# Performance work log

Measured on AMD Instinct MI355X. Metric: run time of the kernel, lower is better.

## Reference

```python
import jax, jax.numpy as jnp
import numpy as np
from jax import lax

N_ITER = 5
SMOOTHNESS_WEIGHT = 1.0
SMOOTHNESS_THETA = 1.0
FILTER_SIZE = 11  # crfseg-style default odd Gaussian filter size


def _gaussian_kernel_1d():
    c = (FILTER_SIZE - 1) / 2.0
    d = jnp.arange(FILTER_SIZE, dtype=jnp.float32) - c
    k = jnp.exp(-(d ** 2) / (2.0 * SMOOTHNESS_THETA ** 2))
    return k / jnp.sum(k)


def _blur(q):
    # q: (B, C, H, W); separable per-channel Gaussian smoothing, 'same' padding
    B, C, H, W = q.shape
    k = _gaussian_kernel_1d()
    r = q.reshape(B * C, 1, H, W)
    dn = ('NCHW', 'OIHW', 'NCHW')
    r = lax.conv_general_dilated(r, k.reshape(1, 1, FILTER_SIZE, 1), (1, 1), 'SAME', dimension_numbers=dn)
    r = lax.conv_general_dilated(r, k.reshape(1, 1, 1, FILTER_SIZE), (1, 1), 'SAME', dimension_numbers=dn)
    return r.reshape(B, C, H, W)


def setup_inputs() -> dict:
    key = jax.random.key(0)
    k1, k2 = jax.random.split(key)
    x = jax.random.normal(k1, (16, 3, 512, 512), dtype=jnp.float32)
    conv_w = jax.random.normal(k2, (2, 3, 3, 3), dtype=jnp.float32) * 0.1
    conv_b = jnp.zeros((2,), dtype=jnp.float32)
    return {"x": x, "conv_w": conv_w, "conv_b": conv_b}


def reference(x, conv_w, conv_b):
    # backbone: simple 3x3 conv producing per-class logits (B, C, H, W)
    dn = ('NCHW', 'OIHW', 'NCHW')
    logits = lax.conv_general_dilated(x, conv_w, (1, 1), 'SAME', dimension_numbers=dn)
    logits = logits + conv_b[None, :, None, None]

    # mean-field CRF: compatibility mu(k,k') = -(k==k') => message = -blur(q)
    unary = logits
    cur = logits
    for _ in range(N_ITER):
        q = jax.nn.softmax(cur, axis=1)
        cur = unary + SMOOTHNESS_WEIGHT * _blur(q)
    return cur
```

## Files before the change

### kernel.cpp

```cpp
#include <hip/hip_runtime.h>

constexpr int BB = 16;
constexpr int HH = 512;
constexpr int WW = 512;
constexpr int HW = HH * WW;
constexpr int NP1 = BB * HW;

using half_t = _Float16;
using half2v = __attribute__((ext_vector_type(2))) _Float16;
using half8v = __attribute__((ext_vector_type(8))) _Float16;

__device__ __forceinline__ half2v hfma2(half2v a, half2v b, half2v c) {
#if __has_builtin(__builtin_elementwise_fma)
    return __builtin_elementwise_fma(a, b, c);
#else
    return a * b + c;
#endif
}

__device__ constexpr float GK[11] = {
    1.4867195147342977e-06f,
    1.3383022576488537e-04f,
    4.4318484119380075e-03f,
    5.3990966513188063e-02f,
    2.4197072451914337e-01f,
    3.9894228040143270e-01f,
    2.4197072451914337e-01f,
    5.3990966513188063e-02f,
    4.4318484119380075e-03f,
    1.3383022576488537e-04f,
    1.4867195147342977e-06f,
};
__device__ constexpr float PFX[6] = {
    0.0f,
    1.4867195147342977e-06f,
    1.3531694527962e-04f,
    4.5671653572176e-03f,
    5.8558131870406e-02f,
    3.0052885638955e-01f,
};

__device__ __forceinline__ float edgeS(int i) {
    float s = 1.f;
    if (i < 5)   s -= PFX[5 - i];
    if (i > 506) s -= PFX[i - 506];
    return s;
}

__device__ __forceinline__ float sig1(float d) {
    d = fminf(fmaxf(d, -30.f), 30.f);
    float e = __expf(d);
    return e * __builtin_amdgcn_rcpf(1.f + e);
}

__device__ __forceinline__ half2v hblur_pk(const half_t* vr, int tid) {
    const unsigned int* vd = (const unsigned int*)vr;
    unsigned int D[7];
#pragma unroll
    for (int k = 0; k < 7; ++k) D[k] = vd[tid + k];
    half2v m01 = half2v{(half_t)0.f, (half_t)0.f};
#pragma unroll
    for (int t = 0; t < 11; ++t) {
        unsigned int P;
        if (t & 1) P = D[(t + 1) >> 1];
        else       P = (D[t >> 1] >> 16) | (D[(t >> 1) + 1] << 16);
        half2v Ph = __builtin_bit_cast(half2v, P);
        half_t kh = (half_t)GK[t];
        half2v kv = half2v{kh, kh};
        m01 = hfma2(kv, Ph, m01);
    }
    return m01;
}

__global__ __launch_bounds__(256) void conv3x3_duq(
    const float* __restrict__ x, const float* __restrict__ w,
    const float* __restrict__ bias, half_t* __restrict__ u0p,
    half_t* __restrict__ dup, half_t* __restrict__ q0p)
{
    int bid = blockIdx.x;
    int sb  = (bid & 7) * 128 + (bid >> 3);
    int t   = sb * 256 + threadIdx.x;
    int b   = t >> 14;
    int rem = t & 16383;
    int y0  = (rem >> 6) << 1;
    int xs  = (rem & 63) << 3;

    float W[54];
#pragma unroll
    for (int i = 0; i < 13; ++i)
        *(float4*)&W[4 * i] = *(const float4*)(w + 4 * i);
    W[52] = w[52];
    W[53] = w[53];
    float b0 = bias[0], b1 = bias[1];

    float acc0[2][8], acc1[2][8];
#pragma unroll
    for (int r = 0; r < 2; ++r)
#pragma unroll
        for (int j = 0; j < 8; ++j) { acc0[r][j] = b0; acc1[r][j] = b1; }

    const float* xb = x + (size_t)b * 3 * HW;
#pragma unroll
    for (int ci = 0; ci < 3; ++ci) {
        const float* xc = xb + ci * HW;
#pragma unroll
        for (int iy = 0; iy < 4; ++iy) {
            int yy = y0 - 1 + iy;
            if (yy < 0 || yy >= HH) continue;
            const float* r = xc + yy * WW;
            float4 cA = *(const float4*)(r + xs);
            float4 cB = *(const float4*)(r + xs + 4);
            float l  = (xs > 0)      ? r[xs - 1] : 0.f;
            float rr = (xs < WW - 8) ? r[xs + 8] : 0.f;
            float v[10] = {l, cA.x, cA.y, cA.z, cA.w,
                           cB.x, cB.y, cB.z, cB.w, rr};
#pragma unroll
            for (int orow = 0; orow < 2; ++orow) {
                int kh = iy - orow;
                if (kh < 0 || kh > 2) continue;
                float w00 = W[ci * 9 + kh * 3 + 0];
                float w01 = W[ci * 9 + kh * 3 + 1];
                float w02 = W[ci * 9 + kh * 3 + 2];
                float w10 = W[27 + ci * 9 + kh * 3 + 0];
                float w11 = W[27 + ci * 9 + kh * 3 + 1];
                float w12 = W[27 + ci * 9 + kh * 3 + 2];
#pragma unroll
                for (int j = 0; j < 8; ++j) {
                    acc0[orow][j] = fmaf(w00, v[j],
                                    fmaf(w01, v[j + 1],
                                    fmaf(w02, v[j + 2], acc0[orow][j])));
                    acc1[orow][j] = fmaf(w10, v[j],
                                    fmaf(w11, v[j + 1],
                                    fmaf(w12, v[j + 2], acc1[orow][j])));
                }
            }
        }
    }
#pragma unroll
    for (int orow = 0; orow < 2; ++orow) {
        size_t o = (size_t)b * HW + (size_t)(y0 + orow) * WW + xs;
        half8v h0, h1, hq;
#pragma unroll
        for (int j = 0; j < 8; ++j) {
            float du = acc1[orow][j] - acc0[orow][j];
            h0[j] = (half_t)acc0[orow][j];
            h1[j] = (half_t)du;
            hq[j] = (half_t)sig1(du);
        }
        *(half8v*)(u0p + o) = h0;
        *(half8v*)(dup + o) = h1;
        *(half8v*)(q0p + o) = hq;
    }
}

__global__ __launch_bounds__(256) void q_iter(
    const half_t* __restrict__ qp, const half_t* __restrict__ dup,
    half_t* __restrict__ qnxt)
{
    __shared__ half_t v[8][528];

    int bid  = blockIdx.x;
    int tile = (bid & 7) * 128 + (bid >> 3);
    int b    = tile >> 6;
    int y0   = (tile & 63) << 3;
    int tid  = threadIdx.x;
    int x0   = tid << 1;

    if (tid < 6) {
#pragma unroll
        for (int r = 0; r < 8; ++r) {
            v[r][tid] = (half_t)0.f;
            v[r][518 + tid] = (half_t)0.f;
        }
    }

    size_t pb = (size_t)b * HW + x0;

    half2v acc[8];
#pragma unroll
    for (int r = 0; r < 8; ++r) acc[r] = half2v{(half_t)0.f, (half_t)0.f};

#pragma unroll
    for (int i = 0; i < 18; ++i) {
        int yy = y0 + i - 5;
        if (yy < 0 || yy >= HH) continue;
        half2v qv = *(const half2v*)(qp + pb + (size_t)yy * WW);
#pragma unroll
        for (int r = 0; r < 8; ++r) {
            int dt = i - r;
            if (dt < 0 || dt > 10) continue;
            half_t kh = (half_t)GK[dt];
            half2v kv = half2v{kh, kh};
            acc[r] = hfma2(kv, qv, acc[r]);
        }
    }
#pragma unroll
    for (int r = 0; r < 8; ++r)
        *(half2v*)(&v[r][6 + x0]) = acc[r];
    __syncthreads();

    float SxA = edgeS(x0), SxB = edgeS(x0 + 1);

#pragma unroll
    for (int r = 0; r < 8; ++r) {
        int yy = y0 + r;
        float Sy = edgeS(yy);

        half2v m01h = hblur_pk(&v[r][0], tid);
        float m0 = (float)m01h[0], m1 = (float)m01h[1];

        size_t po = pb + (size_t)yy * WW;
        half2v duv = *(const half2v*)(dup + po);
        float d0 = (float)duv[0] + fmaf(2.f, m0, -(SxA * Sy));
        float d1 = (float)duv[1] + fmaf(2.f, m1, -(SxB * Sy));

        half2v hq;
        hq[0] = (half_t)sig1(d0);
        hq[1] = (half_t)sig1(d1);
        *(half2v*)(qnxt + po) = hq;
    }
}

__global__ __launch_bounds__(256) void q_final(
    const half_t* __restrict__ qp, const half_t* __restrict__ dup,
    const half_t* __restrict__ u0p, float* __restrict__ outp)
{
    __shared__ half_t v[8][528];

    int bid  = blockIdx.x;
    int tile = (bid & 7) * 128 + (bid >> 3);
    int b    = tile >> 6;
    int y0   = (tile & 63) << 3;
    int tid  = threadIdx.x;
    int x0   = tid << 1;

    if (tid < 6) {
#pragma unroll
        for (int r = 0; r < 8; ++r) {
            v[r][tid] = (half_t)0.f;
            v[r][518 + tid] = (half_t)0.f;
        }
    }

    size_t pb = (size_t)b * HW + x0;

    half2v acc[8];
#pragma unroll
    for (int r = 0; r < 8; ++r) acc[r] = half2v{(half_t)0.f, (half_t)0.f};

#pragma unroll
    for (int i = 0; i < 18; ++i) {
        int yy = y0 + i - 5;
        if (yy < 0 || yy >= HH) continue;
        half2v qv = *(const half2v*)(qp + pb + (size_t)yy * WW);
#pragma unroll
        for (int r = 0; r < 8; ++r) {
            int dt = i - r;
            if (dt < 0 || dt > 10) continue;
            half_t kh = (half_t)GK[dt];
            half2v kv = half2v{kh, kh};
            acc[r] = hfma2(kv, qv, acc[r]);
        }
    }
#pragma unroll
    for (int r = 0; r < 8; ++r)
        *(half2v*)(&v[r][6 + x0]) = acc[r];
    __syncthreads();

    float SxA = edgeS(x0), SxB = edgeS(x0 + 1);

#pragma unroll
    for (int r = 0; r < 8; ++r) {
        int yy = y0 + r;
        float Sy = edgeS(yy);

        half2v m01h = hblur_pk(&v[r][0], tid);
        float m0 = (float)m01h[0], m1 = (float)m01h[1];

        size_t po = pb + (size_t)yy * WW;
        half2v duv = *(const half2v*)(dup + po);
        half2v u0v = *(const half2v*)(u0p + po);
        float dua = (float)duv[0], dub = (float)duv[1];
        float ua  = (float)u0v[0], ub  = (float)u0v[1];

        float S0 = SxA * Sy, S1 = SxB * Sy;
        size_t oo = (size_t)b * 2 * HW + (size_t)yy * WW + x0;
        *(float2*)(outp + oo)      = make_float2(ua + (S0 - m0),
                                                 ub + (S1 - m1));
        *(float2*)(outp + oo + HW) = make_float2((ua + dua) + m0,
                                                 (ub + dub) + m1);
    }
}

extern "C" void kernel_launch(void* const* d_in, const int* in_sizes, int n_in,
                              void* d_out, int out_size, void* d_ws, size_t ws_size,
                              hipStream_t stream) {
    const float* x    = (const float*)d_in[0];
    const float* w    = (const float*)d_in[1];
    const float* bias = (const float*)d_in[2];

    float*  out = (float*)d_out;
    half_t* u0p = (half_t*)d_ws;
    half_t* dup = u0p + NP1;
    half_t* qA  = dup + NP1;
    half_t* qB  = qA + NP1;

    conv3x3_duq<<<1024, 256, 0, stream>>>(x, w, bias, u0p, dup, qA);
    q_iter<<<1024, 256, 0, stream>>>(qA, dup, qB);
    q_iter<<<1024, 256, 0, stream>>>(qB, dup, qA);
    q_iter<<<1024, 256, 0, stream>>>(qA, dup, qB);
    q_iter<<<1024, 256, 0, stream>>>(qB, dup, qA);
    q_final<<<1024, 256, 0, stream>>>(qA, dup, u0p, out);
}
```

Before: 69.57 us.

## Fuse CRF iterations into one persistent kernel with neighbor-tile flag sync

Replaces the four q_iter launches and q_final with a single persistent kernel of 512 blocks. Each block owns a 16-row tile, keeps its q and du rows in registers, and only reads halo rows from global memory after spinning on per-tile flags set by its up and down neighbours. This removes kernel-launch gaps and most of the q/du re-reads, but it relies on all 512 blocks being co-resident to avoid deadlock, and it adds spin-wait and fence overhead.

```diff
diff --git a/kernel.cpp b/kernel.cpp
--- a/kernel.cpp
+++ b/kernel.cpp
@@ -75,9 +75,12 @@
 __global__ __launch_bounds__(256) void conv3x3_duq(
     const float* __restrict__ x, const float* __restrict__ w,
     const float* __restrict__ bias, half_t* __restrict__ u0p,
-    half_t* __restrict__ dup, half_t* __restrict__ q0p)
+    half_t* __restrict__ dup, half_t* __restrict__ q0p,
+    int* __restrict__ flags)
 {
     int bid = blockIdx.x;
+    if (bid < 2) flags[bid * 256 + threadIdx.x] = 0;
+
     int sb  = (bid & 7) * 128 + (bid >> 3);
     int t   = sb * 256 + threadIdx.x;
     int b   = t >> 14;
@@ -153,142 +156,126 @@
     }
 }
 
-__global__ __launch_bounds__(256) void q_iter(
-    const half_t* __restrict__ qp, const half_t* __restrict__ dup,
-    half_t* __restrict__ qnxt)
+__global__ __launch_bounds__(256) void crf_mega(
+    const half_t* __restrict__ q0p, const half_t* __restrict__ dup,
+    const half_t* __restrict__ u0p, half_t* __restrict__ qA,
+    half_t* __restrict__ qB, float* __restrict__ outp,
+    int* flags)
 {
-    __shared__ half_t v[8][528];
+    __shared__ half_t v[16][528];
 
     int bid  = blockIdx.x;
-    int tile = (bid & 7) * 128 + (bid >> 3);
-    int b    = tile >> 6;
-    int y0   = (tile & 63) << 3;
+    int tile = (bid & 7) * 64 + (bid >> 3);
+    int b    = tile >> 5;
+    int yt   = tile & 31;
+    int y0   = yt << 4;
     int tid  = threadIdx.x;
     int x0   = tid << 1;
 
     if (tid < 6) {
 #pragma unroll
-        for (int r = 0; r < 8; ++r) {
+        for (int r = 0; r < 16; ++r) {
             v[r][tid] = (half_t)0.f;
             v[r][518 + tid] = (half_t)0.f;
         }
     }
 
     size_t pb = (size_t)b * HW + x0;
-
-    half2v acc[8];
-#pragma unroll
-    for (int r = 0; r < 8; ++r) acc[r] = half2v{(half_t)0.f, (half_t)0.f};
-
-#pragma unroll
-    for (int i = 0; i < 18; ++i) {
-        int yy = y0 + i - 5;
-        if (yy < 0 || yy >= HH) continue;
-        half2v qv = *(const half2v*)(qp + pb + (size_t)yy * WW);
-#pragma unroll
-        for (int r = 0; r < 8; ++r) {
-            int dt = i - r;
-            if (dt < 0 || dt > 10) continue;
-            half_t kh = (half_t)GK[dt];
-            half2v kv = half2v{kh, kh};
-            acc[r] = hfma2(kv, qv, acc[r]);
-        }
-    }
-#pragma unroll
-    for (int r = 0; r < 8; ++r)
-        *(half2v*)(&v[r][6 + x0]) = acc[r];
-    __syncthreads();
-
     float SxA = edgeS(x0), SxB = edgeS(x0 + 1);
-
-#pragma unroll
-    for (int r = 0; r < 8; ++r) {
-        int yy = y0 + r;
-        float Sy = edgeS(yy);
-
-        half2v m01h = hblur_pk(&v[r][0], tid);
-        float m0 = (float)m01h[0], m1 = (float)m01h[1];
-
-        size_t po = pb + (size_t)yy * WW;
-        half2v duv = *(const half2v*)(dup + po);
-        float d0 = (float)duv[0] + fmaf(2.f, m0, -(SxA * Sy));
-        float d1 = (float)duv[1] + fmaf(2.f, m1, -(SxB * Sy));
-
-        half2v hq;
-        hq[0] = (half_t)sig1(d0);
-        hq[1] = (half_t)sig1(d1);
-        *(half2v*)(qnxt + po) = hq;
-    }
-}
-
-__global__ __launch_bounds__(256) void q_final(
-    const half_t* __restrict__ qp, const half_t* __restrict__ dup,
-    const half_t* __restrict__ u0p, float* __restrict__ outp)
-{
-    __shared__ half_t v[8][528];
-
-    int bid  = blockIdx.x;
-    int tile = (bid & 7) * 128 + (bid >> 3);
-    int b    = tile >> 6;
-    int y0   = (tile & 63) << 3;
-    int tid  = threadIdx.x;
-    int x0   = tid << 1;
-
-    if (tid < 6) {
-#pragma unroll
-        for (int r = 0; r < 8; ++r) {
-            v[r][tid] = (half_t)0.f;
-            v[r][518 + tid] = (half_t)0.f;
-        }
-    }
-
-    size_t pb = (size_t)b * HW + x0;
-
-    half2v acc[8];
-#pragma unroll
-    for (int r = 0; r < 8; ++r) acc[r] = half2v{(half_t)0.f, (half_t)0.f};
-
-#pragma unroll
-    for (int i = 0; i < 18; ++i) {
-        int yy = y0 + i - 5;
-        if (yy < 0 || yy >= HH) continue;
-        half2v qv = *(const half2v*)(qp + pb + (size_t)yy * WW);
-#pragma unroll
-        for (int r = 0; r < 8; ++r) {
-            int dt = i - r;
-            if (dt < 0 || dt > 10) continue;
-            half_t kh = (half_t)GK[dt];
-            half2v kv = half2v{kh, kh};
-            acc[r] = hfma2(kv, qv, acc[r]);
-        }
-    }
-#pragma unroll
-    for (int r = 0; r < 8; ++r)
-        *(half2v*)(&v[r][6 + x0]) = acc[r];
-    __syncthreads();
-
-    float SxA = edgeS(x0), SxB = edgeS(x0 + 1);
-
-#pragma unroll
-    for (int r = 0; r < 8; ++r) {
-        int yy = y0 + r;
-        float Sy = edgeS(yy);
-
-        half2v m01h = hblur_pk(&v[r][0], tid);
-        float m0 = (float)m01h[0], m1 = (float)m01h[1];
-
-        size_t po = pb + (size_t)yy * WW;
-        half2v duv = *(const half2v*)(dup + po);
-        half2v u0v = *(const half2v*)(u0p + po);
-        float dua = (float)duv[0], dub = (float)duv[1];
-        float ua  = (float)u0v[0], ub  = (float)u0v[1];
-
-        float S0 = SxA * Sy, S1 = SxB * Sy;
-        size_t oo = (size_t)b * 2 * HW + (size_t)yy * WW + x0;
-        *(float2*)(outp + oo)      = make_float2(ua + (S0 - m0),
-                                                 ub + (S1 - m1));
-        *(float2*)(outp + oo + HW) = make_float2((ua + dua) + m0,
-                                                 (ub + dub) + m1);
+    bool has_up = (yt > 0), has_dn = (yt < 31);
+
+    half2v q[16], du[16];
+#pragma unroll
+    for (int r = 0; r < 16; ++r) {
+        size_t po = pb + (size_t)(y0 + r) * WW;
+        q[r]  = *(const half2v*)(q0p + po);
+        du[r] = *(const half2v*)(dup + po);
+    }
+
+    for (int j = 1; j <= 5; ++j) {
+        if (j >= 2) {
+            if (tid == 0) {
+                if (has_up)
+                    while (__hip_atomic_load(&flags[tile - 1], __ATOMIC_ACQUIRE,
+                                             __HIP_MEMORY_SCOPE_AGENT) < j - 1)
+                        __builtin_amdgcn_s_sleep(1);
+                if (has_dn)
+                    while (__hip_atomic_load(&flags[tile + 1], __ATOMIC_ACQUIRE,
+                                             __HIP_MEMORY_SCOPE_AGENT) < j - 1)
+                        __builtin_amdgcn_s_sleep(1);
+            }
+            __syncthreads();
+        }
+
+        const half_t* hs = (j == 1) ? q0p : ((j & 1) ? qB : qA);
+
+        half2v acc[16];
+#pragma unroll
+        for (int r = 0; r < 16; ++r) acc[r] = half2v{(half_t)0.f, (half_t)0.f};
+#pragma unroll
+        for (int i = 0; i < 26; ++i) {
+            int yy = y0 + i - 5;
+            if (yy < 0 || yy >= HH) continue;
+            half2v qv;
+            if (i >= 5 && i < 21) qv = q[i - 5];
+            else qv = *(const half2v*)(hs + pb + (size_t)yy * WW);
+#pragma unroll
+            for (int r = 0; r < 16; ++r) {
+                int dt = i - r;
+                if (dt < 0 || dt > 10) continue;
+                half_t kh = (half_t)GK[dt];
+                half2v kv = half2v{kh, kh};
+                acc[r] = hfma2(kv, qv, acc[r]);
+            }
+        }
+
+        __syncthreads();
+#pragma unroll
+        for (int r = 0; r < 16; ++r)
+            *(half2v*)(&v[r][6 + x0]) = acc[r];
+        __syncthreads();
+
+        if (j < 5) {
+            half_t* dst = (j & 1) ? qA : qB;
+#pragma unroll
+            for (int r = 0; r < 16; ++r) {
+                int yy = y0 + r;
+                float Sy = edgeS(yy);
+                half2v m01h = hblur_pk(&v[r][0], tid);
+                float m0 = (float)m01h[0], m1 = (float)m01h[1];
+                float d0 = (float)du[r][0] + fmaf(2.f, m0, -(SxA * Sy));
+                float d1 = (float)du[r][1] + fmaf(2.f, m1, -(SxB * Sy));
+                half2v hq;
+                hq[0] = (half_t)sig1(d0);
+                hq[1] = (half_t)sig1(d1);
+                q[r] = hq;
+                *(half2v*)(dst + pb + (size_t)yy * WW) = hq;
+            }
+            __syncthreads();
+            if (tid == 0) {
+                __threadfence();
+                __hip_atomic_store(&flags[tile], j, __ATOMIC_RELEASE,
+                                   __HIP_MEMORY_SCOPE_AGENT);
+            }
+        } else {
+#pragma unroll
+            for (int r = 0; r < 16; ++r) {
+                int yy = y0 + r;
+                float Sy = edgeS(yy);
+                half2v m01h = hblur_pk(&v[r][0], tid);
+                float m0 = (float)m01h[0], m1 = (float)m01h[1];
+                size_t po = pb + (size_t)yy * WW;
+                half2v u0v = *(const half2v*)(u0p + po);
+                float ua = (float)u0v[0], ub = (float)u0v[1];
+                float dua = (float)du[r][0], dub = (float)du[r][1];
+                float S0 = SxA * Sy, S1 = SxB * Sy;
+                size_t oo = (size_t)b * 2 * HW + (size_t)yy * WW + x0;
+                *(float2*)(outp + oo)      = make_float2(ua + (S0 - m0),
+                                                         ub + (S1 - m1));
+                *(float2*)(outp + oo + HW) = make_float2((ua + dua) + m0,
+                                                         (ub + dub) + m1);
+            }
+        }
     }
 }
 
@@ -302,13 +289,11 @@
     float*  out = (float*)d_out;
     half_t* u0p = (half_t*)d_ws;
     half_t* dup = u0p + NP1;
-    half_t* qA  = dup + NP1;
+    half_t* q0p = dup + NP1;
+    half_t* qA  = q0p + NP1;
     half_t* qB  = qA + NP1;
-
-    conv3x3_duq<<<1024, 256, 0, stream>>>(x, w, bias, u0p, dup, qA);
-    q_iter<<<1024, 256, 0, stream>>>(qA, dup, qB);
-    q_iter<<<1024, 256, 0, stream>>>(qB, dup, qA);
-    q_iter<<<1024, 256, 0, stream>>>(qA, dup, qB);
-    q_iter<<<1024, 256, 0, stream>>>(qB, dup, qA);
-    q_final<<<1024, 256, 0, stream>>>(qA, dup, u0p, out);
-}
+    int*   flags = (int*)(qB + NP1);
+
+    conv3x3_duq<<<1024, 256, 0, stream>>>(x, w, bias, u0p, dup, q0p, flags);
+    crf_mega<<<512, 256, 0, stream>>>(q0p, dup, u0p, qA, qB, out, flags);
+}
```

Result: slower. 182.0 us (+161.6%).
